# Kernel tuning notes

Hardware: AMD Instinct MI355X
Metric: run time of the kernel (lower is better)

## Reference

```python
import jax, jax.numpy as jnp
import numpy as np
import math

EMB = 128
HW = 128

def setup_inputs() -> dict:
    key = jax.random.key(0)
    k_t, k1, k2, k3, k4 = jax.random.split(key, 5)
    B = 8192
    t = jax.random.uniform(k_t, (B,), dtype=jnp.float32)
    s = 1.0 / math.sqrt(EMB)
    W1 = jax.random.uniform(k1, (EMB, EMB), dtype=jnp.float32, minval=-s, maxval=s)
    b1 = jax.random.uniform(k2, (EMB,), dtype=jnp.float32, minval=-s, maxval=s)
    W2 = jax.random.uniform(k3, (EMB, EMB), dtype=jnp.float32, minval=-s, maxval=s)
    b2 = jax.random.uniform(k4, (EMB,), dtype=jnp.float32, minval=-s, maxval=s)
    return {"t": t, "W1": W1, "b1": b1, "W2": W2, "b2": b2}

def reference(t, W1, b1, W2, b2):
    # sinusoidal embedding: 64 log-spaced freqs in [1, 1000]
    freqs = jnp.exp(jnp.linspace(math.log(1.0), math.log(1000.0), EMB // 2)).astype(jnp.float32)
    ang = (2.0 * math.pi) * freqs  # [64]
    phase = t[:, None] * ang[None, :]  # [B, 64]
    emb = jnp.concatenate([jnp.sin(phase), jnp.cos(phase)], axis=-1)  # [B, 128]
    # MLP: Linear -> SiLU -> Linear -> SiLU (torch Linear: x @ W.T + b)
    h = jax.nn.silu(emb @ W1.T + b1)
    h = jax.nn.silu(h @ W2.T + b2)
    # [B,1,1,128] nearest-upsampled to [B,1,128,128]: broadcast along H
    out = jnp.broadcast_to(h[:, None, None, :], (h.shape[0], 1, HW, HW))
    return out
```

## Files before the change

### kernel.cpp

```cpp
#include <hip/hip_runtime.h>
#include <math.h>

typedef float f32x4 __attribute__((ext_vector_type(4)));

__global__ __launch_bounds__(256, 4) void k_fused(
    const float* __restrict__ t,
    const float* __restrict__ W1, const float* __restrict__ b1,
    const float* __restrict__ W2, const float* __restrict__ b2,
    float* __restrict__ out)
{
    __shared__ __attribute__((aligned(16))) float EH[8 * 128];
    __shared__ __attribute__((aligned(16))) float H1[8 * 128];

    const int tid  = threadIdx.x;
    const int base = blockIdx.x * 8;

    const int r = tid & 127;
    const int g = tid >> 7;

    #pragma unroll
    for (int i = 0; i < 2; ++i) {
        int idx = i * 256 + tid;
        int b = idx >> 6, k = idx & 63;
        double a   = (double)k * (6.907755278982137 / 63.0);
        float freq = (float)exp(a);
        float ang  = 6.2831853071795865f * freq;
        float ph   = t[base + b] * ang;
        float sv, cv;
        sincosf(ph, &sv, &cv);
        EH[b * 128 + k]      = sv;
        EH[b * 128 + 64 + k] = cv;
    }
    __syncthreads();

    {
        const f32x4* wp = (const f32x4*)(W1 + r * 128);
        float acc[4];
        float bv = b1[r];
        #pragma unroll
        for (int m = 0; m < 4; ++m) acc[m] = bv;
        #pragma unroll 4
        for (int k4 = 0; k4 < 32; ++k4) {
            f32x4 w = wp[k4];
            #pragma unroll
            for (int m = 0; m < 4; ++m) {
                f32x4 ev = ((const f32x4*)(EH + (g * 4 + m) * 128))[k4];
                acc[m] = fmaf(w.x, ev.x, acc[m]);
                acc[m] = fmaf(w.y, ev.y, acc[m]);
                acc[m] = fmaf(w.z, ev.z, acc[m]);
                acc[m] = fmaf(w.w, ev.w, acc[m]);
            }
        }
        #pragma unroll
        for (int m = 0; m < 4; ++m) {
            float a = acc[m];
            H1[(g * 4 + m) * 128 + r] = a / (1.0f + expf(-a));
        }
    }
    __syncthreads();

    {
        const f32x4* wp = (const f32x4*)(W2 + r * 128);
        float acc[4];
        float bv = b2[r];
        #pragma unroll
        for (int m = 0; m < 4; ++m) acc[m] = bv;
        #pragma unroll 4
        for (int k4 = 0; k4 < 32; ++k4) {
            f32x4 w = wp[k4];
            #pragma unroll
            for (int m = 0; m < 4; ++m) {
                f32x4 ev = ((const f32x4*)(H1 + (g * 4 + m) * 128))[k4];
                acc[m] = fmaf(w.x, ev.x, acc[m]);
                acc[m] = fmaf(w.y, ev.y, acc[m]);
                acc[m] = fmaf(w.z, ev.z, acc[m]);
                acc[m] = fmaf(w.w, ev.w, acc[m]);
            }
        }
        #pragma unroll
        for (int m = 0; m < 4; ++m) {
            float a = acc[m];
            EH[(g * 4 + m) * 128 + r] = a / (1.0f + expf(-a));
        }
    }
    __syncthreads();

    #pragma unroll
    for (int m = 0; m < 8; ++m) {
        f32x4 v = *(const f32x4*)&EH[m * 128 + (tid & 31) * 4];
        f32x4* d = (f32x4*)(out + (size_t)(base + m) * 16384);
        #pragma unroll
        for (int c = 0; c < 16; ++c) {
            d[c * 256 + tid] = v;
        }
    }
}

extern "C" void kernel_launch(void* const* d_in, const int* in_sizes, int n_in,
                              void* d_out, int out_size, void* d_ws, size_t ws_size,
                              hipStream_t stream) {
    const float* t  = (const float*)d_in[0];
    const float* W1 = (const float*)d_in[1];
    const float* b1 = (const float*)d_in[2];
    const float* W2 = (const float*)d_in[3];
    const float* b2 = (const float*)d_in[4];
    float* out = (float*)d_out;
    const int B = in_sizes[0];

    k_fused<<<B / 8, 256, 0, stream>>>(t, W1, b1, W2, b2, out);
}
```

Before: 555.5 us.

## Shrink blocks to one wavefront handling four rows with two outputs per lane

Each block is now a single 64-thread wavefront that processes 4 batch rows instead of 8. Each lane computes two output features for all four rows in both linear layers, and the grid doubles. The kernel is dominated by a 512 MB output write, so the intent is to raise the number of independent blocks and cut synchronisation cost relative to the store traffic. In exchange, weight loads per row double and each block issues less parallel write traffic.

```diff
diff --git a/kernel.cpp b/kernel.cpp
--- a/kernel.cpp
+++ b/kernel.cpp
@@ -3,95 +3,106 @@
 
 typedef float f32x4 __attribute__((ext_vector_type(4)));
 
-__global__ __launch_bounds__(256, 4) void k_fused(
+__global__ __launch_bounds__(64) void k_fused(
     const float* __restrict__ t,
     const float* __restrict__ W1, const float* __restrict__ b1,
     const float* __restrict__ W2, const float* __restrict__ b2,
     float* __restrict__ out)
 {
-    __shared__ __attribute__((aligned(16))) float EH[8 * 128];
-    __shared__ __attribute__((aligned(16))) float H1[8 * 128];
+    __shared__ __attribute__((aligned(16))) float E [4 * 128];
+    __shared__ __attribute__((aligned(16))) float H1[4 * 128];
 
-    const int tid  = threadIdx.x;
-    const int base = blockIdx.x * 8;
+    const int l    = threadIdx.x;
+    const int base = blockIdx.x * 4;
 
-    const int r = tid & 127;
-    const int g = tid >> 7;
-
-    #pragma unroll
-    for (int i = 0; i < 2; ++i) {
-        int idx = i * 256 + tid;
-        int b = idx >> 6, k = idx & 63;
-        double a   = (double)k * (6.907755278982137 / 63.0);
+    {
+        double a   = (double)l * (6.907755278982137 / 63.0);
         float freq = (float)exp(a);
         float ang  = 6.2831853071795865f * freq;
-        float ph   = t[base + b] * ang;
-        float sv, cv;
-        sincosf(ph, &sv, &cv);
-        EH[b * 128 + k]      = sv;
-        EH[b * 128 + 64 + k] = cv;
-    }
-    __syncthreads();
-
-    {
-        const f32x4* wp = (const f32x4*)(W1 + r * 128);
-        float acc[4];
-        float bv = b1[r];
         #pragma unroll
-        for (int m = 0; m < 4; ++m) acc[m] = bv;
-        #pragma unroll 4
-        for (int k4 = 0; k4 < 32; ++k4) {
-            f32x4 w = wp[k4];
-            #pragma unroll
-            for (int m = 0; m < 4; ++m) {
-                f32x4 ev = ((const f32x4*)(EH + (g * 4 + m) * 128))[k4];
-                acc[m] = fmaf(w.x, ev.x, acc[m]);
-                acc[m] = fmaf(w.y, ev.y, acc[m]);
-                acc[m] = fmaf(w.z, ev.z, acc[m]);
-                acc[m] = fmaf(w.w, ev.w, acc[m]);
-            }
-        }
-        #pragma unroll
-        for (int m = 0; m < 4; ++m) {
-            float a = acc[m];
-            H1[(g * 4 + m) * 128 + r] = a / (1.0f + expf(-a));
+        for (int b = 0; b < 4; ++b) {
+            float ph = t[base + b] * ang;
+            float sv, cv;
+            sincosf(ph, &sv, &cv);
+            E[b * 128 + l]      = sv;
+            E[b * 128 + 64 + l] = cv;
         }
     }
     __syncthreads();
 
     {
-        const f32x4* wp = (const f32x4*)(W2 + r * 128);
-        float acc[4];
-        float bv = b2[r];
+        const f32x4* w0 = (const f32x4*)(W1 + l * 128);
+        const f32x4* w1 = (const f32x4*)(W1 + (l + 64) * 128);
+        float acc[2][4];
+        float bv0 = b1[l], bv1 = b1[l + 64];
         #pragma unroll
-        for (int m = 0; m < 4; ++m) acc[m] = bv;
-        #pragma unroll 4
+        for (int b = 0; b < 4; ++b) { acc[0][b] = bv0; acc[1][b] = bv1; }
+        #pragma unroll 8
         for (int k4 = 0; k4 < 32; ++k4) {
-            f32x4 w = wp[k4];
+            f32x4 wa = w0[k4];
+            f32x4 wb = w1[k4];
             #pragma unroll
-            for (int m = 0; m < 4; ++m) {
-                f32x4 ev = ((const f32x4*)(H1 + (g * 4 + m) * 128))[k4];
-                acc[m] = fmaf(w.x, ev.x, acc[m]);
-                acc[m] = fmaf(w.y, ev.y, acc[m]);
-                acc[m] = fmaf(w.z, ev.z, acc[m]);
-                acc[m] = fmaf(w.w, ev.w, acc[m]);
+            for (int b = 0; b < 4; ++b) {
+                f32x4 ev = ((const f32x4*)(E + b * 128))[k4];
+                acc[0][b] = fmaf(wa.x, ev.x, acc[0][b]);
+                acc[0][b] = fmaf(wa.y, ev.y, acc[0][b]);
+                acc[0][b] = fmaf(wa.z, ev.z, acc[0][b]);
+                acc[0][b] = fmaf(wa.w, ev.w, acc[0][b]);
+                acc[1][b] = fmaf(wb.x, ev.x, acc[1][b]);
+                acc[1][b] = fmaf(wb.y, ev.y, acc[1][b]);
+                acc[1][b] = fmaf(wb.z, ev.z, acc[1][b]);
+                acc[1][b] = fmaf(wb.w, ev.w, acc[1][b]);
             }
         }
         #pragma unroll
-        for (int m = 0; m < 4; ++m) {
-            float a = acc[m];
-            EH[(g * 4 + m) * 128 + r] = a / (1.0f + expf(-a));
+        for (int b = 0; b < 4; ++b) {
+            float a0 = acc[0][b], a1 = acc[1][b];
+            H1[b * 128 + l]      = a0 / (1.0f + expf(-a0));
+            H1[b * 128 + 64 + l] = a1 / (1.0f + expf(-a1));
+        }
+    }
+    __syncthreads();
+
+    {
+        const f32x4* w0 = (const f32x4*)(W2 + l * 128);
+        const f32x4* w1 = (const f32x4*)(W2 + (l + 64) * 128);
+        float acc[2][4];
+        float bv0 = b2[l], bv1 = b2[l + 64];
+        #pragma unroll
+        for (int b = 0; b < 4; ++b) { acc[0][b] = bv0; acc[1][b] = bv1; }
+        #pragma unroll 8
+        for (int k4 = 0; k4 < 32; ++k4) {
+            f32x4 wa = w0[k4];
+            f32x4 wb = w1[k4];
+            #pragma unroll
+            for (int b = 0; b < 4; ++b) {
+                f32x4 ev = ((const f32x4*)(H1 + b * 128))[k4];
+                acc[0][b] = fmaf(wa.x, ev.x, acc[0][b]);
+                acc[0][b] = fmaf(wa.y, ev.y, acc[0][b]);
+                acc[0][b] = fmaf(wa.z, ev.z, acc[0][b]);
+                acc[0][b] = fmaf(wa.w, ev.w, acc[0][b]);
+                acc[1][b] = fmaf(wb.x, ev.x, acc[1][b]);
+                acc[1][b] = fmaf(wb.y, ev.y, acc[1][b]);
+                acc[1][b] = fmaf(wb.z, ev.z, acc[1][b]);
+                acc[1][b] = fmaf(wb.w, ev.w, acc[1][b]);
+            }
+        }
+        #pragma unroll
+        for (int b = 0; b < 4; ++b) {
+            float a0 = acc[0][b], a1 = acc[1][b];
+            E[b * 128 + l]      = a0 / (1.0f + expf(-a0));
+            E[b * 128 + 64 + l] = a1 / (1.0f + expf(-a1));
         }
     }
     __syncthreads();
 
     #pragma unroll
-    for (int m = 0; m < 8; ++m) {
-        f32x4 v = *(const f32x4*)&EH[m * 128 + (tid & 31) * 4];
-        f32x4* d = (f32x4*)(out + (size_t)(base + m) * 16384);
+    for (int b = 0; b < 4; ++b) {
+        f32x4 v  = *(const f32x4*)&E[b * 128 + (l & 31) * 4];
+        f32x4* d = (f32x4*)(out + (size_t)(base + b) * 16384);
         #pragma unroll
-        for (int c = 0; c < 16; ++c) {
-            d[c * 256 + tid] = v;
+        for (int c = 0; c < 64; ++c) {
+            d[c * 64 + l] = v;
         }
     }
 }
@@ -107,5 +118,5 @@
     float* out = (float*)d_out;
     const int B = in_sizes[0];
 
-    k_fused<<<B / 8, 256, 0, stream>>>(t, W1, b1, W2, b2, out);
+    k_fused<<<B / 4, 64, 0, stream>>>(t, W1, b1, W2, b2, out);
 }
```

Result: no change. 560.0 us (+0.8%).
